# Kernel optimization log

Hardware: AMD Instinct MI355X
Metric: run time of the kernel (lower is better)

Reference implementation:

```python
import jax, jax.numpy as jnp
import numpy as np
import math

D_MODEL = 1024
N_HEADS = 16
D_K = D_MODEL // N_HEADS
R_TYPES = 8
B, S = 2, 2048


def setup_inputs() -> dict:
    key = jax.random.key(0)
    ks = jax.random.split(key, 12)
    sc = 0.02
    return {
        "x": jax.random.normal(ks[0], (B, S, D_MODEL), jnp.float32),
        "Wq": jax.random.normal(ks[1], (D_MODEL, D_MODEL), jnp.float32) * sc,
        "bq": jax.random.normal(ks[2], (D_MODEL,), jnp.float32) * sc,
        "Wk": jax.random.normal(ks[3], (D_MODEL, D_MODEL), jnp.float32) * sc,
        "bk": jax.random.normal(ks[4], (D_MODEL,), jnp.float32) * sc,
        "Wv": jax.random.normal(ks[5], (D_MODEL, D_MODEL), jnp.float32) * sc,
        "bv": jax.random.normal(ks[6], (D_MODEL,), jnp.float32) * sc,
        "Wo": jax.random.normal(ks[7], (D_MODEL, D_MODEL), jnp.float32) * sc,
        "bo": jax.random.normal(ks[8], (D_MODEL,), jnp.float32) * sc,
        "resource_bias": jax.random.normal(ks[9], (N_HEADS, R_TYPES, R_TYPES), jnp.float32),
        "resource_mask": jax.random.randint(ks[10], (B, S), 0, R_TYPES, jnp.int32),
        "attention_mask": jnp.ones((B, S), jnp.int32),
    }


def reference(x, resource_mask, attention_mask, Wq, bq, Wk, bk, Wv, bv, Wo, bo, resource_bias):
    # torch nn.Linear: y = x @ W.T + b
    def lin(h, W, b):
        return jnp.einsum("bsd,ed->bse", h, W) + b

    def split_heads(t):  # [B,S,D] -> [B,H,S,d_k]
        return t.reshape(B, S, N_HEADS, D_K).transpose(0, 2, 1, 3)

    Q = split_heads(lin(x, Wq, bq))
    K = split_heads(lin(x, Wk, bk))
    V = split_heads(lin(x, Wv, bv))

    scores = jnp.einsum("bhid,bhjd->bhij", Q, K) / math.sqrt(D_K)  # [B,H,S,S]

    # vectorized resource-bias gather: bias[h, r_i, r_j] added to scores[b,h,i,j]
    r = resource_mask.astype(jnp.int32)  # values guaranteed < R_TYPES
    # resource_bias[:, r[b,i], r[b,j]] -> [B,H,S,S]
    bias = resource_bias[:, r[:, :, None], r[:, None, :]]  # [H,B,S,S]
    scores = scores + bias.transpose(1, 0, 2, 3)

    mask = attention_mask[:, None, None, :]  # [B,1,1,S] broadcast to [B,H,S,S]
    scores = jnp.where(mask == 0, jnp.float32(-1e9), scores)

    attn = jax.nn.softmax(scores, axis=-1)  # dropout is identity in eval
    out = jnp.einsum("bhij,bhjd->bhid", attn, V)
    out = out.transpose(0, 2, 1, 3).reshape(B, S, D_MODEL)
    return jnp.einsum("bsd,ed->bse", out, Wo) + bo
```

## Files before the change

### kernel.cpp

```cpp
#include <hip/hip_runtime.h>
#include <cstdint>

#define D_MODEL 1024
#define NHEADS  16
#define DKH     64
#define SEQ     2048
#define NBATCH  2
#define MROWS   (NBATCH*SEQ)
#define RTYPES  8
#define LOG2E   1.44269504f

typedef __bf16 bf16;
typedef __bf16 bf16x4v __attribute__((ext_vector_type(4)));
typedef __bf16 bf16x8v __attribute__((ext_vector_type(8)));
typedef float  f32x4v  __attribute__((ext_vector_type(4)));

typedef unsigned int __attribute__((address_space(1))) as1_u32;
typedef unsigned int __attribute__((address_space(3))) as3_u32;

static __device__ __forceinline__ void gload_lds16(const void* g, void* l) {
  __builtin_amdgcn_global_load_lds((const as1_u32*)(uintptr_t)g,
                                   (as3_u32*)(uintptr_t)l, 16, 0, 0);
}

static __device__ __forceinline__ f32x4v mfma16(bf16x8v a, bf16x8v b, f32x4v c) {
  return __builtin_amdgcn_mfma_f32_16x16x32_bf16(a, b, c, 0, 0, 0);
}

__global__ void convert_kernel(const float* __restrict__ x,  const float* __restrict__ wq,
                               const float* __restrict__ wk, const float* __restrict__ wv,
                               const float* __restrict__ wo,
                               bf16* __restrict__ xb,  bf16* __restrict__ wqb,
                               bf16* __restrict__ wkb, bf16* __restrict__ wvb,
                               bf16* __restrict__ wob,
                               const float* __restrict__ rbias,
                               const int* __restrict__ rmask,
                               const int* __restrict__ amask,
                               float* __restrict__ biasg)
{
  int idx = blockIdx.x*256 + threadIdx.x;
  if (idx < 1048576){
    float4 v = ((const float4*)x)[idx];
    bf16x4v o = { (bf16)v.x, (bf16)v.y, (bf16)v.z, (bf16)v.w };
    ((bf16x4v*)xb)[idx] = o;
  } else if (idx < 2097152){
    int r = (idx - 1048576) >> 18;
    int i = (idx - 1048576) & 262143;
    const float* src; bf16* dst;
    if (r == 0)      { src = wq; dst = wqb; }
    else if (r == 1) { src = wk; dst = wkb; }
    else if (r == 2) { src = wv; dst = wvb; }
    else             { src = wo; dst = wob; }
    float4 v = ((const float4*)src)[i];
    bf16x4v o = { (bf16)v.x, (bf16)v.y, (bf16)v.z, (bf16)v.w };
    ((bf16x4v*)dst)[i] = o;
  } else {
    int i = idx - 2097152;
    #pragma unroll
    for (int bb=0; bb<NBATCH; bb++){
      int id2 = bb*(NHEADS*RTYPES*SEQ) + i;
      int j  = id2 & (SEQ-1);
      int t  = (id2 >> 11) & 7;
      int hh = (id2 >> 14) & 15;
      int rj = rmask[bb*SEQ + j];
      float am = amask[bb*SEQ + j] ? 0.f : -1e9f;
      biasg[id2] = (rbias[(hh*RTYPES + t)*RTYPES + rj] + am) * LOG2E;
    }
  }
}

struct GemmOuts { const bf16* W[3]; const float* bia[3]; void* out[3]; };

template<int FUSED>
__global__ __launch_bounds__(256, 3) void gemm_bt_kernel(
    const bf16* __restrict__ A, GemmOuts args, float qscale)
{
  const int K  = D_MODEL;
  const int z  = FUSED ? blockIdx.z : 0;
  const bf16*  Bw   = args.W[z];
  const float* bias = args.bia[z];
  void* outp        = args.out[z];
  const float scale = (FUSED && z==0) ? qscale : 1.0f;

  const int n0 = blockIdx.x*128, m0 = blockIdx.y*128;
  const int tid = threadIdx.x;
  const int w = tid>>6, lane = tid&63, g = lane>>4, c = lane&15;
  const int wm = w>>1, wn = w&1;

  __shared__ __align__(16) bf16 a_lds[2][128*32];
  __shared__ __align__(16) bf16 b_lds[2][128*32];

  const f32x4v fzero = {0.f,0.f,0.f,0.f};
  f32x4v acc[4][4];
  for (int i=0;i<4;i++) for (int j=0;j<4;j++) acc[i][j] = fzero;

  const int srow = tid>>2, sc8 = tid&3;

  auto STAGE = [&](int k0, int nb){
    gload_lds16(A  + (size_t)(m0+srow)*K     + k0 + sc8*8, &a_lds[nb][(w*64)*8]);
    gload_lds16(Bw + (size_t)(n0+srow)*K     + k0 + sc8*8, &b_lds[nb][(w*64)*8]);
    gload_lds16(A  + (size_t)(m0+64+srow)*K  + k0 + sc8*8, &a_lds[nb][(256 + w*64)*8]);
    gload_lds16(Bw + (size_t)(n0+64+srow)*K  + k0 + sc8*8, &b_lds[nb][(256 + w*64)*8]);
  };

  auto COMPUTE = [&](int nb){
    bf16x8v af[4], bfv[4];
    #pragma unroll
    for (int mt=0;mt<4;mt++)
      af[mt] = *(const bf16x8v*)&a_lds[nb][(wm*64 + mt*16 + c)*32 + g*8];
    #pragma unroll
    for (int nt=0;nt<4;nt++)
      bfv[nt] = *(const bf16x8v*)&b_lds[nb][(wn*64 + nt*16 + c)*32 + g*8];
    #pragma unroll
    for (int mt=0;mt<4;mt++)
      #pragma unroll
      for (int nt=0;nt<4;nt++)
        acc[mt][nt] = mfma16(af[mt], bfv[nt], acc[mt][nt]);
  };

  STAGE(0, 0);
  __syncthreads();
  int cur = 0;
  for (int k0=32; k0<K; k0+=32){
    STAGE(k0, cur^1);
    COMPUTE(cur);
    __syncthreads();
    cur ^= 1;
  }
  COMPUTE(cur);

  #pragma unroll
  for (int mt=0;mt<4;mt++){
    #pragma unroll
    for (int nt=0;nt<4;nt++){
      if (FUSED && z == 2){
        int m = m0 + wm*64 + mt*16 + g*4;
        int n = n0 + wn*64 + nt*16 + c;
        int bb=m>>11, s=m&2047, hh=n>>6, dk=n&63;
        float bn = bias[n];
        bf16x4v ov;
        #pragma unroll
        for (int r=0;r<4;r++) ov[r] = (bf16)(acc[mt][nt][r] + bn);
        *(bf16x4v*)&((bf16*)outp)[(((size_t)bb*NHEADS+hh)*DKH + dk)*SEQ + s] = ov;
      } else {
        #pragma unroll
        for (int r=0;r<4;r++){
          int m = m0 + wm*64 + mt*16 + g*4 + r;
          int n = n0 + wn*64 + nt*16 + c;
          float v = acc[mt][nt][r] + bias[n];
          if (FUSED){
            v *= scale;
            int bb=m>>11, s=m&2047, hh=n>>6, dk=n&63;
            ((bf16*)outp)[(((size_t)bb*NHEADS+hh)*SEQ + s)*DKH + dk] = (bf16)v;
          } else {
            ((float*)outp)[(size_t)m*D_MODEL + n] = v;
          }
        }
      }
    }
  }
}

__global__ __launch_bounds__(512, 4) void attn4_kernel(
    const bf16* __restrict__ Qg, const bf16* __restrict__ Kg,
    const bf16* __restrict__ Vtg, const float* __restrict__ biasg,
    const int* __restrict__ rmask, bf16* __restrict__ Og)
{
  const int b = blockIdx.z, h = blockIdx.y, q0 = blockIdx.x*128;
  const int tid = threadIdx.x;
  const int w = tid>>6, lane = tid&63, g = lane>>4, c = lane&15;
  const int bh = b*NHEADS + h;
  const int NT = SEQ/64;

  __shared__ __align__(16) bf16  k_lds[3][64*64];
  __shared__ __align__(16) bf16  vt_lds[3][64*64];
  __shared__ __align__(16) float bias_lds[3][8*64];

  const int qrow = q0 + w*16 + c;
  const bf16* qptr = Qg + ((size_t)bh*SEQ + qrow)*DKH;
  bf16x8v qf[2];
  qf[0] = *(const bf16x8v*)(qptr + g*8);
  qf[1] = *(const bf16x8v*)(qptr + 32 + g*8);

  const int tq = rmask[b*SEQ + qrow];
  const int tsw = (tq&7) << 2;

  bf16x8v ones;
  #pragma unroll
  for (int i=0;i<8;i++) ones[i] = (bf16)1.0f;

  f32x4v oacc[4];
  #pragma unroll
  for (int dt=0;dt<4;dt++) oacc[dt] = {0.f,0.f,0.f,0.f};
  f32x4v lacc = {0.f,0.f,0.f,0.f};
  float mrow = -1e30f;

  const int rho = tid>>3;
  const int c8s = (tid&7) ^ (rho&7);
  const int jlog = ((rho>>4)&1)*32 + ((rho>>2)&3)*8 + ((rho>>5)&1)*4 + (rho&3);

  auto STAGE = [&](int j0, int nb){
    gload_lds16(Kg  + ((size_t)bh*SEQ + j0 + jlog)*DKH + (c8s<<3), &k_lds[nb][w*512]);
    gload_lds16(Vtg + ((size_t)bh*DKH + rho)*SEQ + j0 + (c8s<<3),  &vt_lds[nb][w*512]);
    if (w < 2){
      int chunk = w*64 + lane;
      int tcls = chunk>>4, c16 = chunk&15;
      int jsw = (c16<<2) ^ ((tcls&7)<<2);
      gload_lds16(biasg + ((size_t)(bh*RTYPES + tcls))*SEQ + j0 + jsw, &bias_lds[nb][w*256]);
    }
  };

  auto COMPUTE = [&](int nb){
    const char*  kb_ = (const char*)k_lds[nb];
    const char*  vb_ = (const char*)vt_lds[nb];
    const float* bb_ = &bias_lds[nb][0];

    f32x4v s[4];
    #pragma unroll
    for (int nt=0;nt<4;nt++){
      int jb = (nt&1)*32 + g*8 + (nt>>1)*4;
      s[nt] = *(const f32x4v*)&bb_[tq*64 + (jb ^ tsw)];
      #pragma unroll
      for (int kt=0;kt<2;kt++){
        int row = nt*16 + c;
        bf16x8v kf = *(const bf16x8v*)(kb_ + row*128 + ((kt*64 + g*16) ^ ((row&7)<<4)));
        s[nt] = mfma16(kf, qf[kt], s[nt]);
      }
    }

    float a0 = fmaxf(fmaxf(s[0][0],s[0][1]),s[0][2]);
    float a1 = fmaxf(fmaxf(s[0][3],s[1][0]),s[1][1]);
    float a2 = fmaxf(fmaxf(s[1][2],s[1][3]),s[2][0]);
    float a3 = fmaxf(fmaxf(s[2][1],s[2][2]),s[2][3]);
    float a4 = fmaxf(fmaxf(s[3][0],s[3][1]),s[3][2]);
    float mx = fmaxf(fmaxf(fmaxf(a0,a1),a2), fmaxf(fmaxf(a3,a4),s[3][3]));
    mx = fmaxf(mx, __shfl_xor(mx, 16));
    mx = fmaxf(mx, __shfl_xor(mx, 32));

    if (!__all(mx - mrow <= 8.0f)){
      float mnew = fmaxf(mrow, mx);
      float scl = exp2f(mrow - mnew);
      #pragma unroll
      for (int dt=0;dt<4;dt++)
        #pragma unroll
        for (int r=0;r<4;r++) oacc[dt][r] *= scl;
      #pragma unroll
      for (int r=0;r<4;r++) lacc[r] *= scl;
      mrow = mnew;
    }

    #pragma unroll
    for (int nt=0;nt<4;nt++)
      #pragma unroll
      for (int r=0;r<4;r++)
        s[nt][r] = exp2f(s[nt][r] - mrow);

    bf16x8v pa[2];
    #pragma unroll
    for (int kt=0;kt<2;kt++){
      pa[kt][0]=(bf16)s[kt][0];   pa[kt][1]=(bf16)s[kt][1];
      pa[kt][2]=(bf16)s[kt][2];   pa[kt][3]=(bf16)s[kt][3];
      pa[kt][4]=(bf16)s[kt+2][0]; pa[kt][5]=(bf16)s[kt+2][1];
      pa[kt][6]=(bf16)s[kt+2][2]; pa[kt][7]=(bf16)s[kt+2][3];
    }

    lacc = mfma16(ones, pa[0], lacc);
    lacc = mfma16(ones, pa[1], lacc);

    #pragma unroll
    for (int dt=0;dt<4;dt++){
      #pragma unroll
      for (int kt=0;kt<2;kt++){
        int vr = dt*16 + c;
        bf16x8v vf = *(const bf16x8v*)(vb_ + vr*128 + ((kt*64 + g*16) ^ ((vr&7)<<4)));
        oacc[dt] = mfma16(vf, pa[kt], oacc[dt]);
      }
    }
  };

  STAGE(0, 0);
  STAGE(64, 1);
  if (w < 2) asm volatile("s_waitcnt vmcnt(3)" ::: "memory");
  else       asm volatile("s_waitcnt vmcnt(2)" ::: "memory");
  __builtin_amdgcn_s_barrier();

  int cur = 0;
  for (int t=0; t<NT; ++t){
    if (t+2 < NT){
      int nb2 = cur+2; if (nb2 >= 3) nb2 -= 3;
      STAGE((t+2)*64, nb2);
    }
    COMPUTE(cur);
    if (t+2 < NT){
      if (w < 2) asm volatile("s_waitcnt vmcnt(3)" ::: "memory");
      else       asm volatile("s_waitcnt vmcnt(2)" ::: "memory");
    } else {
      asm volatile("s_waitcnt vmcnt(0)" ::: "memory");
    }
    __builtin_amdgcn_s_barrier();
    cur = (cur+1 == 3) ? 0 : cur+1;
  }

  const float inv = 1.0f / lacc[0];
  #pragma unroll
  for (int dt=0;dt<4;dt++){
    bf16x4v ov;
    #pragma unroll
    for (int r=0;r<4;r++) ov[r] = (bf16)(oacc[dt][r] * inv);
    int row = q0 + w*16 + c;
    int col = h*DKH + dt*16 + g*4;
    *(bf16x4v*)&Og[(size_t)(b*SEQ + row)*D_MODEL + col] = ov;
  }
}

extern "C" void kernel_launch(void* const* d_in, const int* in_sizes, int n_in,
                              void* d_out, int out_size, void* d_ws, size_t ws_size,
                              hipStream_t stream)
{
  (void)in_sizes; (void)n_in; (void)out_size; (void)ws_size;
  const float* x     = (const float*)d_in[0];
  const float* Wq    = (const float*)d_in[1];
  const float* bq    = (const float*)d_in[2];
  const float* Wk    = (const float*)d_in[3];
  const float* bk    = (const float*)d_in[4];
  const float* Wv    = (const float*)d_in[5];
  const float* bv    = (const float*)d_in[6];
  const float* Wo    = (const float*)d_in[7];
  const float* bo    = (const float*)d_in[8];
  const float* rbias = (const float*)d_in[9];
  const int*   rmask = (const int*)d_in[10];
  const int*   amask = (const int*)d_in[11];
  float* out = (float*)d_out;

  char* ws = (char*)d_ws;
  bf16*  xb    = (bf16*)(ws);
  bf16*  wqb   = (bf16*)(ws + (8u<<20));
  bf16*  wkb   = (bf16*)(ws + (10u<<20));
  bf16*  wvb   = (bf16*)(ws + (12u<<20));
  bf16*  wob   = (bf16*)(ws + (14u<<20));
  bf16*  qb    = (bf16*)(ws + (16u<<20));
  bf16*  kb    = (bf16*)(ws + (24u<<20));
  bf16*  vtb   = (bf16*)(ws + (32u<<20));
  bf16*  aob   = (bf16*)(ws + (40u<<20));
  float* biasg = (float*)(ws + (48u<<20));

  convert_kernel<<<9216, 256, 0, stream>>>(x,Wq,Wk,Wv,Wo, xb,wqb,wkb,wvb,wob,
                                           rbias, rmask, amask, biasg);

  GemmOuts qkv;
  qkv.W[0]=wqb; qkv.W[1]=wkb; qkv.W[2]=wvb;
  qkv.bia[0]=bq; qkv.bia[1]=bk; qkv.bia[2]=bv;
  qkv.out[0]=qb; qkv.out[1]=kb; qkv.out[2]=vtb;
  gemm_bt_kernel<1><<<dim3(D_MODEL/128, MROWS/128, 3), 256, 0, stream>>>(xb, qkv, 0.125f*LOG2E);

  attn4_kernel<<<dim3(SEQ/128, NHEADS, NBATCH), 512, 0, stream>>>(qb, kb, vtb, biasg, rmask, aob);

  GemmOuts og;
  og.W[0]=wob; og.W[1]=wob; og.W[2]=wob;
  og.bia[0]=bo; og.bia[1]=bo; og.bia[2]=bo;
  og.out[0]=out; og.out[1]=out; og.out[2]=out;
  gemm_bt_kernel<0><<<dim3(D_MODEL/128, MROWS/128), 256, 0, stream>>>(aob, og, 1.0f);
}
```

Baseline: 138.9 us.

## Switch attention to 32x32x16 MFMA with 32 query rows per wave

Rewrites the attention kernel to use 32x32x16 bf16 MFMA tiles, so each wave handles 32 query rows and the block shrinks from 8 to 4 waves covering the same 128 queries. The staging, bias-swizzle and LDS read patterns are reworked to match the new fragment layouts, and the vmcnt waits are adjusted because each thread now issues more loads per stage. The aim is to cut LDS fragment reads and MFMA instruction count per unit of work and to need fewer cross-lane reductions. In exchange each wave holds more accumulator registers, and fewer waves per block may reduce latency hiding.

```diff
diff --git a/kernel.cpp b/kernel.cpp
--- a/kernel.cpp
+++ b/kernel.cpp
@@ -14,6 +14,8 @@
 typedef __bf16 bf16x4v __attribute__((ext_vector_type(4)));
 typedef __bf16 bf16x8v __attribute__((ext_vector_type(8)));
 typedef float  f32x4v  __attribute__((ext_vector_type(4)));
+typedef float  f32x8v  __attribute__((ext_vector_type(8)));
+typedef float  f32x16v __attribute__((ext_vector_type(16)));
 
 typedef unsigned int __attribute__((address_space(1))) as1_u32;
 typedef unsigned int __attribute__((address_space(3))) as3_u32;
@@ -25,6 +27,9 @@
 
 static __device__ __forceinline__ f32x4v mfma16(bf16x8v a, bf16x8v b, f32x4v c) {
   return __builtin_amdgcn_mfma_f32_16x16x32_bf16(a, b, c, 0, 0, 0);
+}
+static __device__ __forceinline__ f32x16v mfma32(bf16x8v a, bf16x8v b, f32x16v c) {
+  return __builtin_amdgcn_mfma_f32_32x32x16_bf16(a, b, c, 0, 0, 0);
 }
 
 __global__ void convert_kernel(const float* __restrict__ x,  const float* __restrict__ wq,
@@ -161,14 +166,15 @@
   }
 }
 
-__global__ __launch_bounds__(512, 4) void attn4_kernel(
+__global__ __launch_bounds__(256, 2) void attn5_kernel(
     const bf16* __restrict__ Qg, const bf16* __restrict__ Kg,
     const bf16* __restrict__ Vtg, const float* __restrict__ biasg,
     const int* __restrict__ rmask, bf16* __restrict__ Og)
 {
   const int b = blockIdx.z, h = blockIdx.y, q0 = blockIdx.x*128;
   const int tid = threadIdx.x;
-  const int w = tid>>6, lane = tid&63, g = lane>>4, c = lane&15;
+  const int w = tid>>6, lane = tid&63;
+  const int q5 = lane&31, hi = lane>>5;
   const int bh = b*NHEADS + h;
   const int NT = SEQ/64;
 
@@ -176,37 +182,54 @@
   __shared__ __align__(16) bf16  vt_lds[3][64*64];
   __shared__ __align__(16) float bias_lds[3][8*64];
 
-  const int qrow = q0 + w*16 + c;
+  const int qrow = q0 + w*32 + q5;
   const bf16* qptr = Qg + ((size_t)bh*SEQ + qrow)*DKH;
-  bf16x8v qf[2];
-  qf[0] = *(const bf16x8v*)(qptr + g*8);
-  qf[1] = *(const bf16x8v*)(qptr + 32 + g*8);
+  bf16x8v qf[4];
+  #pragma unroll
+  for (int kc=0;kc<4;kc++)
+    qf[kc] = *(const bf16x8v*)(qptr + kc*16 + hi*8);
 
   const int tq = rmask[b*SEQ + qrow];
-  const int tsw = (tq&7) << 2;
+
+  int boff[2][4];
+  #pragma unroll
+  for (int nt=0;nt<2;nt++){
+    const int j00 = nt*32 + hi*8;
+    boff[nt][0] = tq*64 + ((j00 +  0) ^ (tq*8));
+    boff[nt][1] = tq*64 + ((j00 +  4) ^ (tq*8));
+    boff[nt][2] = tq*64 + ((j00 + 16) ^ (tq*8));
+    boff[nt][3] = tq*64 + ((j00 + 20) ^ (tq*8));
+  }
 
   bf16x8v ones;
   #pragma unroll
   for (int i=0;i<8;i++) ones[i] = (bf16)1.0f;
 
-  f32x4v oacc[4];
-  #pragma unroll
-  for (int dt=0;dt<4;dt++) oacc[dt] = {0.f,0.f,0.f,0.f};
-  f32x4v lacc = {0.f,0.f,0.f,0.f};
+  f32x16v oacc[2];
+  #pragma unroll
+  for (int dt=0;dt<2;dt++)
+    #pragma unroll
+    for (int r=0;r<16;r++) oacc[dt][r] = 0.f;
+  f32x16v lacc;
+  #pragma unroll
+  for (int r=0;r<16;r++) lacc[r] = 0.f;
   float mrow = -1e30f;
 
-  const int rho = tid>>3;
-  const int c8s = (tid&7) ^ (rho&7);
-  const int jlog = ((rho>>4)&1)*32 + ((rho>>2)&3)*8 + ((rho>>5)&1)*4 + (rho&3);
-
   auto STAGE = [&](int j0, int nb){
-    gload_lds16(Kg  + ((size_t)bh*SEQ + j0 + jlog)*DKH + (c8s<<3), &k_lds[nb][w*512]);
-    gload_lds16(Vtg + ((size_t)bh*DKH + rho)*SEQ + j0 + (c8s<<3),  &vt_lds[nb][w*512]);
+    #pragma unroll
+    for (int i=0;i<2;i++){
+      const int chunk = i*256 + tid;
+      const int p = chunk>>3, c8 = chunk&7;
+      const int jsrc = (p & 32) + (p & 3) + (((p>>3)&1)<<2) + (((p>>2)&1)<<3) + (p & 16);
+      const int dsrc = (c8 ^ (p&7)) << 3;
+      gload_lds16(Kg  + ((size_t)bh*SEQ + j0 + jsrc)*DKH + dsrc, &k_lds[nb][(i*256 + w*64)*8]);
+      gload_lds16(Vtg + ((size_t)bh*DKH + p)*SEQ + j0 + dsrc,    &vt_lds[nb][(i*256 + w*64)*8]);
+    }
     if (w < 2){
-      int chunk = w*64 + lane;
-      int tcls = chunk>>4, c16 = chunk&15;
-      int jsw = (c16<<2) ^ ((tcls&7)<<2);
-      gload_lds16(biasg + ((size_t)(bh*RTYPES + tcls))*SEQ + j0 + jsw, &bias_lds[nb][w*256]);
+      const int chunk = w*64 + lane;
+      const int t = chunk>>4, c16 = chunk&15;
+      const int jsw = (c16<<2) ^ (t<<3);
+      gload_lds16(biasg + ((size_t)(bh*RTYPES + t))*SEQ + j0 + jsw, &bias_lds[nb][w*256]);
     }
   };
 
@@ -215,73 +238,74 @@
     const char*  vb_ = (const char*)vt_lds[nb];
     const float* bb_ = &bias_lds[nb][0];
 
-    f32x4v s[4];
-    #pragma unroll
-    for (int nt=0;nt<4;nt++){
-      int jb = (nt&1)*32 + g*8 + (nt>>1)*4;
-      s[nt] = *(const f32x4v*)&bb_[tq*64 + (jb ^ tsw)];
-      #pragma unroll
-      for (int kt=0;kt<2;kt++){
-        int row = nt*16 + c;
-        bf16x8v kf = *(const bf16x8v*)(kb_ + row*128 + ((kt*64 + g*16) ^ ((row&7)<<4)));
-        s[nt] = mfma16(kf, qf[kt], s[nt]);
+    f32x16v s[2];
+    #pragma unroll
+    for (int nt=0;nt<2;nt++){
+      f32x4v b0 = *(const f32x4v*)&bb_[boff[nt][0]];
+      f32x4v b1 = *(const f32x4v*)&bb_[boff[nt][1]];
+      f32x4v b2 = *(const f32x4v*)&bb_[boff[nt][2]];
+      f32x4v b3 = *(const f32x4v*)&bb_[boff[nt][3]];
+      f32x8v h0 = __builtin_shufflevector(b0, b1, 0,1,2,3,4,5,6,7);
+      f32x8v h1 = __builtin_shufflevector(b2, b3, 0,1,2,3,4,5,6,7);
+      s[nt] = __builtin_shufflevector(h0, h1, 0,1,2,3,4,5,6,7,8,9,10,11,12,13,14,15);
+      #pragma unroll
+      for (int kc=0;kc<4;kc++){
+        const int row = nt*32 + q5;
+        bf16x8v kf = *(const bf16x8v*)(kb_ + row*128 + ((kc*32 + hi*16) ^ ((row&7)<<4)));
+        s[nt] = mfma32(kf, qf[kc], s[nt]);
       }
     }
 
-    float a0 = fmaxf(fmaxf(s[0][0],s[0][1]),s[0][2]);
-    float a1 = fmaxf(fmaxf(s[0][3],s[1][0]),s[1][1]);
-    float a2 = fmaxf(fmaxf(s[1][2],s[1][3]),s[2][0]);
-    float a3 = fmaxf(fmaxf(s[2][1],s[2][2]),s[2][3]);
-    float a4 = fmaxf(fmaxf(s[3][0],s[3][1]),s[3][2]);
-    float mx = fmaxf(fmaxf(fmaxf(a0,a1),a2), fmaxf(fmaxf(a3,a4),s[3][3]));
-    mx = fmaxf(mx, __shfl_xor(mx, 16));
+    float mx = s[0][0];
+    #pragma unroll
+    for (int r=1;r<16;r++) mx = fmaxf(mx, s[0][r]);
+    #pragma unroll
+    for (int r=0;r<16;r++) mx = fmaxf(mx, s[1][r]);
     mx = fmaxf(mx, __shfl_xor(mx, 32));
 
     if (!__all(mx - mrow <= 8.0f)){
       float mnew = fmaxf(mrow, mx);
       float scl = exp2f(mrow - mnew);
       #pragma unroll
-      for (int dt=0;dt<4;dt++)
+      for (int dt=0;dt<2;dt++)
         #pragma unroll
-        for (int r=0;r<4;r++) oacc[dt][r] *= scl;
-      #pragma unroll
-      for (int r=0;r<4;r++) lacc[r] *= scl;
+        for (int r=0;r<16;r++) oacc[dt][r] *= scl;
+      #pragma unroll
+      for (int r=0;r<16;r++) lacc[r] *= scl;
       mrow = mnew;
     }
 
     #pragma unroll
-    for (int nt=0;nt<4;nt++)
-      #pragma unroll
-      for (int r=0;r<4;r++)
+    for (int nt=0;nt<2;nt++)
+      #pragma unroll
+      for (int r=0;r<16;r++)
         s[nt][r] = exp2f(s[nt][r] - mrow);
 
-    bf16x8v pa[2];
-    #pragma unroll
-    for (int kt=0;kt<2;kt++){
-      pa[kt][0]=(bf16)s[kt][0];   pa[kt][1]=(bf16)s[kt][1];
-      pa[kt][2]=(bf16)s[kt][2];   pa[kt][3]=(bf16)s[kt][3];
-      pa[kt][4]=(bf16)s[kt+2][0]; pa[kt][5]=(bf16)s[kt+2][1];
-      pa[kt][6]=(bf16)s[kt+2][2]; pa[kt][7]=(bf16)s[kt+2][3];
-    }
-
-    lacc = mfma16(ones, pa[0], lacc);
-    lacc = mfma16(ones, pa[1], lacc);
-
-    #pragma unroll
-    for (int dt=0;dt<4;dt++){
-      #pragma unroll
-      for (int kt=0;kt<2;kt++){
-        int vr = dt*16 + c;
-        bf16x8v vf = *(const bf16x8v*)(vb_ + vr*128 + ((kt*64 + g*16) ^ ((vr&7)<<4)));
-        oacc[dt] = mfma16(vf, pa[kt], oacc[dt]);
+    bf16x8v pa[4];
+    #pragma unroll
+    for (int m=0;m<4;m++)
+      #pragma unroll
+      for (int e=0;e<8;e++)
+        pa[m][e] = (bf16)s[m>>1][e + (m&1)*8];
+
+    #pragma unroll
+    for (int m=0;m<4;m++) lacc = mfma32(ones, pa[m], lacc);
+
+    #pragma unroll
+    for (int dt=0;dt<2;dt++){
+      #pragma unroll
+      for (int m=0;m<4;m++){
+        const int row = dt*32 + q5;
+        bf16x8v vf = *(const bf16x8v*)(vb_ + row*128 + ((m*32 + hi*16) ^ ((row&7)<<4)));
+        oacc[dt] = mfma32(vf, pa[m], oacc[dt]);
       }
     }
   };
 
   STAGE(0, 0);
   STAGE(64, 1);
-  if (w < 2) asm volatile("s_waitcnt vmcnt(3)" ::: "memory");
-  else       asm volatile("s_waitcnt vmcnt(2)" ::: "memory");
+  if (w < 2) asm volatile("s_waitcnt vmcnt(5)" ::: "memory");
+  else       asm volatile("s_waitcnt vmcnt(4)" ::: "memory");
   __builtin_amdgcn_s_barrier();
 
   int cur = 0;
@@ -292,8 +316,8 @@
     }
     COMPUTE(cur);
     if (t+2 < NT){
-      if (w < 2) asm volatile("s_waitcnt vmcnt(3)" ::: "memory");
-      else       asm volatile("s_waitcnt vmcnt(2)" ::: "memory");
+      if (w < 2) asm volatile("s_waitcnt vmcnt(5)" ::: "memory");
+      else       asm volatile("s_waitcnt vmcnt(4)" ::: "memory");
     } else {
       asm volatile("s_waitcnt vmcnt(0)" ::: "memory");
     }
@@ -303,13 +327,15 @@
 
   const float inv = 1.0f / lacc[0];
   #pragma unroll
-  for (int dt=0;dt<4;dt++){
-    bf16x4v ov;
-    #pragma unroll
-    for (int r=0;r<4;r++) ov[r] = (bf16)(oacc[dt][r] * inv);
-    int row = q0 + w*16 + c;
-    int col = h*DKH + dt*16 + g*4;
-    *(bf16x4v*)&Og[(size_t)(b*SEQ + row)*D_MODEL + col] = ov;
+  for (int dt=0;dt<2;dt++){
+    #pragma unroll
+    for (int rq=0;rq<4;rq++){
+      bf16x4v ov;
+      #pragma unroll
+      for (int k=0;k<4;k++) ov[k] = (bf16)(oacc[dt][rq*4+k] * inv);
+      const int d = dt*32 + 8*rq + 4*hi;
+      *(bf16x4v*)&Og[(size_t)(b*SEQ + qrow)*D_MODEL + h*DKH + d] = ov;
+    }
   }
 }
 
@@ -353,7 +379,7 @@
   qkv.out[0]=qb; qkv.out[1]=kb; qkv.out[2]=vtb;
   gemm_bt_kernel<1><<<dim3(D_MODEL/128, MROWS/128, 3), 256, 0, stream>>>(xb, qkv, 0.125f*LOG2E);
 
-  attn4_kernel<<<dim3(SEQ/128, NHEADS, NBATCH), 512, 0, stream>>>(qb, kb, vtb, biasg, rmask, aob);
+  attn5_kernel<<<dim3(SEQ/128, NHEADS, NBATCH), 256, 0, stream>>>(qb, kb, vtb, biasg, rmask, aob);
 
   GemmOuts og;
   og.W[0]=wob; og.W[1]=wob; og.W[2]=wob;
```

Result: no change. 136.9 us (-1.4%).
